# Performance work log

Measured on AMD Instinct MI355X. Metric: run time of the kernel, lower is better.

Reference implementation:

```python
import jax, jax.numpy as jnp
import numpy as np

N = 100000      # nodes
E = 3200000     # directed edges
IN = 512
H = 32          # hidden width fixed by the module
OUT = 64
EPS = 1e-5      # BatchNorm1d default eps


def setup_inputs() -> dict:
    key = jax.random.key(0)
    ks = jax.random.split(key, 10)
    x = jax.random.normal(ks[0], (N, IN), dtype=jnp.float32)
    edge_index = jax.random.randint(ks[1], (2, E), 0, N, dtype=jnp.int32)
    # GCNConv params (Linear weight + bias)
    W1 = jax.random.normal(ks[2], (IN, H), dtype=jnp.float32) / np.sqrt(IN)
    b1 = jnp.zeros((H,), dtype=jnp.float32)
    W2 = jax.random.normal(ks[3], (H, OUT), dtype=jnp.float32) / np.sqrt(H)
    b2 = jnp.zeros((OUT,), dtype=jnp.float32)
    # BatchNorm1d(32) params + running stats (eval mode)
    gamma = jax.random.normal(ks[4], (H,), dtype=jnp.float32) * 0.1 + 1.0
    beta = jax.random.normal(ks[5], (H,), dtype=jnp.float32) * 0.1
    running_mean = jax.random.normal(ks[6], (H,), dtype=jnp.float32) * 0.1
    running_var = jax.random.uniform(ks[7], (H,), dtype=jnp.float32, minval=0.5, maxval=1.5)
    return {"x": x, "edge_index": edge_index, "W1": W1, "b1": b1,
            "W2": W2, "b2": b2, "gamma": gamma, "beta": beta,
            "running_mean": running_mean, "running_var": running_var}


def _gcn_norm(edge_index):
    # PyG GCNConv default: add self-loops, symmetric normalization.
    src0, dst0 = edge_index[0], edge_index[1]
    loops = jnp.arange(N, dtype=edge_index.dtype)
    src = jnp.concatenate([src0, loops])
    dst = jnp.concatenate([dst0, loops])
    deg = jax.ops.segment_sum(jnp.ones_like(dst, dtype=jnp.float32), dst, num_segments=N)
    dinv = jnp.where(deg > 0, jax.lax.rsqrt(deg), 0.0)
    norm = dinv[src] * dinv[dst]  # [E+N]
    return src, dst, norm


def _gcn_conv(h, src, dst, norm, b):
    # gather -> scale -> scatter-add, then bias
    msg = h[src] * norm[:, None]
    agg = jax.ops.segment_sum(msg, dst, num_segments=N)
    return agg + b


def reference(x, edge_index, W1, b1, W2, b2, gamma, beta, running_mean, running_var):
    src, dst, norm = _gcn_norm(edge_index)
    h = _gcn_conv(x @ W1, src, dst, norm, b1)              # [N, 32]
    h = (h - running_mean) * jax.lax.rsqrt(running_var + EPS) * gamma + beta
    h = jax.nn.relu(h)
    # dropout is identity in eval mode
    out = _gcn_conv(h @ W2, src, dst, norm, b2)            # [N, 64]
    return out
```

## Files before the change

### kernel.cpp

```cpp
#include <hip/hip_runtime.h>
#include <hip/hip_fp16.h>

#define N_NODES 100000
#define E_EDGES 3200000
#define IN_F 512
#define H_F 32
#define OUT_F 64
#define BN_EPS 1e-5f
#define NBINS 1563
#define CHUNK 16384

struct H8 { __half2 h[4]; };
typedef _Float16 f16x8 __attribute__((ext_vector_type(8)));
typedef float    f32x4 __attribute__((ext_vector_type(4)));

__global__ __launch_bounds__(256) void k_prep(const float* __restrict__ gamma,
                                              const float* __restrict__ beta,
                                              const float* __restrict__ rm,
                                              const float* __restrict__ rv,
                                              const float* __restrict__ b1,
                                              float* __restrict__ scale,
                                              float* __restrict__ shift,
                                              unsigned* __restrict__ binCnt,
                                              unsigned* __restrict__ binPos) {
    int t = blockIdx.x * 256 + threadIdx.x;
    if (t < NBINS) { binCnt[t] = 0u; binPos[t] = 0u; }
    if (blockIdx.x == 0 && threadIdx.x < H_F) {
        int k = threadIdx.x;
        float s = gamma[k] * rsqrtf(rv[k] + BN_EPS);
        scale[k] = s;
        shift[k] = (b1[k] - rm[k]) * s + beta[k];
    }
}

__global__ __launch_bounds__(256) void k_wt(const float* __restrict__ W1,
                                            __half* __restrict__ w1t) {
    int t = blockIdx.x * 256 + threadIdx.x;
    if (t < IN_F * H_F) {
        int k = t >> 5, c = t & 31;
        w1t[c * IN_F + k] = __float2half(W1[t]);
    }
}

__global__ __launch_bounds__(256) void k_hist(const int* __restrict__ dst,
                                              unsigned* __restrict__ binCnt) {
    __shared__ unsigned h[NBINS];
    for (int i = threadIdx.x; i < NBINS; i += 256) h[i] = 0;
    __syncthreads();
    const int stride = 256 * 512;
    int e = blockIdx.x * 256 + threadIdx.x;
    for (; e + 3 * stride < E_EDGES; e += 4 * stride) {
        unsigned d0 = (unsigned)dst[e];
        unsigned d1 = (unsigned)dst[e + stride];
        unsigned d2 = (unsigned)dst[e + 2 * stride];
        unsigned d3 = (unsigned)dst[e + 3 * stride];
        atomicAdd(&h[d0 >> 6], 1u);
        atomicAdd(&h[d1 >> 6], 1u);
        atomicAdd(&h[d2 >> 6], 1u);
        atomicAdd(&h[d3 >> 6], 1u);
    }
    for (; e < E_EDGES; e += stride)
        atomicAdd(&h[((unsigned)dst[e]) >> 6], 1u);
    __syncthreads();
    for (int i = threadIdx.x; i < NBINS; i += 256) {
        unsigned v = h[i];
        if (v) atomicAdd(&binCnt[i], v);
    }
}

__global__ __launch_bounds__(256) void k_scanbins(const unsigned* __restrict__ binCnt,
                                                  unsigned* __restrict__ binOff) {
    __shared__ unsigned carry;
    __shared__ unsigned wtot[4];
    if (threadIdx.x == 0) carry = 0;
    __syncthreads();
    int lane = threadIdx.x & 63, wid = threadIdx.x >> 6;
    for (int base = 0; base < NBINS; base += 256) {
        int i = base + (int)threadIdx.x;
        unsigned v = (i < NBINS) ? binCnt[i] : 0u;
        unsigned xs = v;
#pragma unroll
        for (int s = 1; s < 64; s <<= 1) {
            unsigned t = __shfl_up(xs, s, 64);
            if (lane >= s) xs += t;
        }
        if (lane == 63) wtot[wid] = xs;
        __syncthreads();
        unsigned wbase = 0, tot = 0;
#pragma unroll
        for (int w = 0; w < 4; ++w) { if (w < wid) wbase += wtot[w]; tot += wtot[w]; }
        if (i < NBINS) binOff[i] = carry + wbase + xs - v;
        __syncthreads();
        if (threadIdx.x == 0) carry += tot;
        __syncthreads();
    }
}

__global__ __launch_bounds__(256) void k_binfill(const int* __restrict__ src,
                                                 const int* __restrict__ dst,
                                                 const unsigned* __restrict__ binOff,
                                                 unsigned* __restrict__ binPos,
                                                 unsigned* __restrict__ packed) {
    __shared__ unsigned h[NBINS];
    for (int i = threadIdx.x; i < NBINS; i += 256) h[i] = 0;
    __syncthreads();
    int e0 = blockIdx.x * CHUNK;
    int e1 = min(e0 + CHUNK, E_EDGES);
    for (int e = e0 + threadIdx.x; e < e1; e += 256)
        atomicAdd(&h[((unsigned)dst[e]) >> 6], 1u);
    __syncthreads();
    for (int i = threadIdx.x; i < NBINS; i += 256) {
        unsigned c = h[i];
        h[i] = c ? atomicAdd(&binPos[i], c) : 0u;
    }
    __syncthreads();
    for (int e = e0 + threadIdx.x; e < e1; e += 256) {
        unsigned s = (unsigned)src[e];
        unsigned d = (unsigned)dst[e];
        unsigned bin = d >> 6;
        unsigned pos = atomicAdd(&h[bin], 1u);
        packed[binOff[bin] + pos] = ((d & 63u) << 17) | s;
    }
}

__global__ __launch_bounds__(256) void k_sortbin(const unsigned* __restrict__ binOff,
                                                 const unsigned* __restrict__ binCnt,
                                                 const unsigned* __restrict__ packed,
                                                 unsigned* __restrict__ off,
                                                 unsigned* __restrict__ deg,
                                                 float* __restrict__ dinv,
                                                 unsigned* __restrict__ csr) {
    __shared__ unsigned cnt[64];
    __shared__ unsigned cur[64];
    int bin = blockIdx.x;
    if (threadIdx.x < 64) cnt[threadIdx.x] = 0;
    __syncthreads();
    unsigned base = binOff[bin], len = binCnt[bin];
    for (unsigned j = threadIdx.x; j < len; j += 256)
        atomicAdd(&cnt[packed[base + j] >> 17], 1u);
    __syncthreads();
    if (threadIdx.x < 64) {
        unsigned v = cnt[threadIdx.x];
        unsigned xs = v;
#pragma unroll
        for (int s = 1; s < 64; s <<= 1) {
            unsigned t = __shfl_up(xs, s, 64);
            if ((int)threadIdx.x >= s) xs += t;
        }
        unsigned loc = xs - v;
        cur[threadIdx.x] = loc;
        int node = bin * 64 + (int)threadIdx.x;
        if (node < N_NODES) {
            off[node]  = base + loc;
            deg[node]  = v;
            dinv[node] = rsqrtf((float)v + 1.0f);
        }
    }
    __syncthreads();
    for (unsigned j = threadIdx.x; j < len; j += 256) {
        unsigned p = packed[base + j];
        unsigned pos = atomicAdd(&cur[p >> 17], 1u);
        csr[base + pos] = p & 0x1FFFFu;
    }
}

__global__ __launch_bounds__(256) void k_gemm1(const float* __restrict__ x,
                                               const __half* __restrict__ w1t,
                                               const float* __restrict__ dinv,
                                               __half* __restrict__ xw16) {
    __shared__ _Float16 wsT[32][520];
    for (int i = threadIdx.x; i < 32 * 64; i += 256) {
        int c = i >> 6, k8 = i & 63;
        *(uint4*)&wsT[c][k8 * 8] = *(const uint4*)(w1t + c * IN_F + k8 * 8);
    }
    __syncthreads();

    const int wt = threadIdx.x >> 6;
    const int l  = threadIdx.x & 63;
    const int lr = l & 15;
    const int lk = l >> 4;
    const int row0 = blockIdx.x * 64 + wt * 16;
    int arow = row0 + lr;
    if (arow >= N_NODES) arow = N_NODES - 1;
    const float* xp = x + (size_t)arow * IN_F + lk * 8;

    f32x4 acc0 = {0.f, 0.f, 0.f, 0.f};
    f32x4 acc1 = {0.f, 0.f, 0.f, 0.f};
#pragma unroll 4
    for (int k0 = 0; k0 < IN_F; k0 += 32) {
        float4 xa = *(const float4*)(xp + k0);
        float4 xb = *(const float4*)(xp + k0 + 4);
        f16x8 a;
        a[0] = (_Float16)xa.x; a[1] = (_Float16)xa.y;
        a[2] = (_Float16)xa.z; a[3] = (_Float16)xa.w;
        a[4] = (_Float16)xb.x; a[5] = (_Float16)xb.y;
        a[6] = (_Float16)xb.z; a[7] = (_Float16)xb.w;
        f16x8 b0 = *(const f16x8*)&wsT[lr][k0 + lk * 8];
        f16x8 b1 = *(const f16x8*)&wsT[16 + lr][k0 + lk * 8];
        acc0 = __builtin_amdgcn_mfma_f32_16x16x32_f16(a, b0, acc0, 0, 0, 0);
        acc1 = __builtin_amdgcn_mfma_f32_16x16x32_f16(a, b1, acc1, 0, 0, 0);
    }
#pragma unroll
    for (int r = 0; r < 4; ++r) {
        int orow = row0 + lk * 4 + r;
        if (orow < N_NODES) {
            float dv = dinv[orow];
            xw16[(size_t)orow * H_F + lr]      = __float2half(acc0[r] * dv);
            xw16[(size_t)orow * H_F + 16 + lr] = __float2half(acc1[r] * dv);
        }
    }
}

__device__ inline void acc8(float* acc, float4 raw) {
    const __half2* h = (const __half2*)&raw;
#pragma unroll
    for (int j = 0; j < 4; ++j) {
        float2 f = __half22float2(h[j]);
        acc[2 * j]     += f.x;
        acc[2 * j + 1] += f.y;
    }
}

__global__ __launch_bounds__(256) void k_gather1(const unsigned* __restrict__ off,
                                                 const unsigned* __restrict__ deg,
                                                 const unsigned* __restrict__ csr,
                                                 const __half* __restrict__ xw16,
                                                 const float* __restrict__ dinv,
                                                 const float* __restrict__ scale,
                                                 const float* __restrict__ shift,
                                                 __half* __restrict__ hs16) {
    int lane  = threadIdx.x & 63;
    int ll    = lane & 31;
    int g     = ll >> 2;
    int q     = ll & 3;
    int d = blockIdx.x * 8 + ((threadIdx.x >> 6) << 1) + (lane >> 5);
    const unsigned* cp = csr + off[d];
    unsigned n = deg[d];
    float acc[8] = {};
    unsigned i = g;
    for (; i + 24 < n; i += 32) {
        unsigned s0 = cp[i], s1 = cp[i + 8], s2 = cp[i + 16], s3 = cp[i + 24];
        float4 r0 = *(const float4*)(xw16 + (size_t)s0 * H_F + q * 8);
        float4 r1 = *(const float4*)(xw16 + (size_t)s1 * H_F + q * 8);
        float4 r2 = *(const float4*)(xw16 + (size_t)s2 * H_F + q * 8);
        float4 r3 = *(const float4*)(xw16 + (size_t)s3 * H_F + q * 8);
        acc8(acc, r0); acc8(acc, r1); acc8(acc, r2); acc8(acc, r3);
    }
    for (; i < n; i += 8) {
        float4 r = *(const float4*)(xw16 + (size_t)cp[i] * H_F + q * 8);
        acc8(acc, r);
    }
#pragma unroll
    for (int st = 4; st <= 16; st <<= 1)
#pragma unroll
        for (int j = 0; j < 8; ++j)
            acc[j] += __shfl_xor(acc[j], st, 64);
    if (g == 0) {
        float dv = dinv[d];
        float sf[8];
        {
            float4 raw = *(const float4*)(xw16 + (size_t)d * H_F + q * 8);
            const __half2* h = (const __half2*)&raw;
#pragma unroll
            for (int j = 0; j < 4; ++j) {
                float2 f = __half22float2(h[j]);
                sf[2 * j] = f.x; sf[2 * j + 1] = f.y;
            }
        }
        float scf[8], shf[8];
        *(float4*)scf       = *(const float4*)(scale + q * 8);
        *(float4*)(scf + 4) = *(const float4*)(scale + q * 8 + 4);
        *(float4*)shf       = *(const float4*)(shift + q * 8);
        *(float4*)(shf + 4) = *(const float4*)(shift + q * 8 + 4);
        H8 o;
#pragma unroll
        for (int j = 0; j < 4; ++j) {
            float a0 = (acc[2 * j]     + sf[2 * j])     * dv;
            float a1 = (acc[2 * j + 1] + sf[2 * j + 1]) * dv;
            float h0 = fmaxf(fmaf(a0, scf[2 * j],     shf[2 * j]),     0.f) * dv;
            float h1 = fmaxf(fmaf(a1, scf[2 * j + 1], shf[2 * j + 1]), 0.f) * dv;
            o.h[j] = __floats2half2_rn(h0, h1);
        }
        *(H8*)(hs16 + (size_t)d * H_F + q * 8) = o;
    }
}

__global__ __launch_bounds__(256) void k_gather2(const unsigned* __restrict__ off,
                                                 const unsigned* __restrict__ deg,
                                                 const unsigned* __restrict__ csr,
                                                 const __half* __restrict__ hs16,
                                                 const float* __restrict__ dinv,
                                                 const float* __restrict__ W2,
                                                 const float* __restrict__ b2,
                                                 float* __restrict__ out) {
    __shared__ float ws[H_F * OUT_F];
    __shared__ float bs[OUT_F];
    for (int i = threadIdx.x; i < H_F * OUT_F; i += 256) ws[i] = W2[i];
    if (threadIdx.x < OUT_F) bs[threadIdx.x] = b2[threadIdx.x];
    __syncthreads();
    int lane  = threadIdx.x & 63;
    int ll    = lane & 31;
    int g     = ll >> 2;
    int q     = ll & 3;
    int d = blockIdx.x * 8 + ((threadIdx.x >> 6) << 1) + (lane >> 5);
    const unsigned* cp = csr + off[d];
    unsigned n = deg[d];
    float acc[8] = {};
    unsigned i = g;
    for (; i + 24 < n; i += 32) {
        unsigned s0 = cp[i], s1 = cp[i + 8], s2 = cp[i + 16], s3 = cp[i + 24];
        float4 r0 = *(const float4*)(hs16 + (size_t)s0 * H_F + q * 8);
        float4 r1 = *(const float4*)(hs16 + (size_t)s1 * H_F + q * 8);
        float4 r2 = *(const float4*)(hs16 + (size_t)s2 * H_F + q * 8);
        float4 r3 = *(const float4*)(hs16 + (size_t)s3 * H_F + q * 8);
        acc8(acc, r0); acc8(acc, r1); acc8(acc, r2); acc8(acc, r3);
    }
    for (; i < n; i += 8) {
        float4 r = *(const float4*)(hs16 + (size_t)cp[i] * H_F + q * 8);
        acc8(acc, r);
    }
#pragma unroll
    for (int st = 4; st <= 16; st <<= 1)
#pragma unroll
        for (int j = 0; j < 8; ++j)
            acc[j] += __shfl_xor(acc[j], st, 64);
    float tv[8];
#pragma unroll
    for (int j = 0; j < 8; ++j) tv[j] = 0.f;
    if (g == 0) {
        float dv = dinv[d];
        float4 raw = *(const float4*)(hs16 + (size_t)d * H_F + q * 8);
        const __half2* h = (const __half2*)&raw;
#pragma unroll
        for (int j = 0; j < 4; ++j) {
            float2 f = __half22float2(h[j]);
            tv[2 * j]     = (acc[2 * j]     + f.x) * dv;
            tv[2 * j + 1] = (acc[2 * j + 1] + f.y) * dv;
        }
    }
    float o0 = bs[ll], o1 = bs[ll + 32];
#pragma unroll
    for (int k = 0; k < H_F; ++k) {
        float a = __shfl(tv[k & 7], k >> 3, 32);
        o0 = fmaf(a, ws[k * OUT_F + ll],      o0);
        o1 = fmaf(a, ws[k * OUT_F + ll + 32], o1);
    }
    out[(size_t)d * OUT_F + ll]      = o0;
    out[(size_t)d * OUT_F + ll + 32] = o1;
}

extern "C" void kernel_launch(void* const* d_in, const int* in_sizes, int n_in,
                              void* d_out, int out_size, void* d_ws, size_t ws_size,
                              hipStream_t stream) {
    const float* x     = (const float*)d_in[0];
    const int*   ei    = (const int*)d_in[1];
    const float* W1    = (const float*)d_in[2];
    const float* b1    = (const float*)d_in[3];
    const float* W2    = (const float*)d_in[4];
    const float* b2    = (const float*)d_in[5];
    const float* gamma = (const float*)d_in[6];
    const float* beta  = (const float*)d_in[7];
    const float* rm    = (const float*)d_in[8];
    const float* rv    = (const float*)d_in[9];
    float* out = (float*)d_out;

    const int* src = ei;
    const int* dst = ei + E_EDGES;

    __half*   xw16   = (__half*)d_ws;
    __half*   hs16   = xw16 + (size_t)N_NODES * H_F;
    unsigned* packed = (unsigned*)d_ws;
    unsigned* csr    = (unsigned*)(hs16 + (size_t)N_NODES * H_F);
    float*    dinv   = (float*)(csr + E_EDGES);
    unsigned* off    = (unsigned*)(dinv + N_NODES);
    unsigned* deg    = off + N_NODES;
    float*    scale  = (float*)(deg + N_NODES);
    float*    shift  = scale + H_F;
    unsigned* binCnt = (unsigned*)(shift + H_F);
    unsigned* binPos = binCnt + NBINS;
    unsigned* binOff = binPos + NBINS;
    __half*   w1t    = (__half*)(binOff + NBINS);

    k_prep<<<(NBINS + 255) / 256, 256, 0, stream>>>(gamma, beta, rm, rv, b1,
                                                    scale, shift, binCnt, binPos);
    k_wt<<<(IN_F * H_F + 255) / 256, 256, 0, stream>>>(W1, w1t);
    k_hist<<<512, 256, 0, stream>>>(dst, binCnt);
    k_scanbins<<<1, 256, 0, stream>>>(binCnt, binOff);
    k_binfill<<<(E_EDGES + CHUNK - 1) / CHUNK, 256, 0, stream>>>(src, dst, binOff, binPos, packed);
    k_sortbin<<<NBINS, 256, 0, stream>>>(binOff, binCnt, packed, off, deg, dinv, csr);

    k_gemm1<<<(N_NODES + 63) / 64, 256, 0, stream>>>(x, w1t, dinv, xw16);
    k_gather1<<<N_NODES / 8, 256, 0, stream>>>(off, deg, csr, xw16, dinv, scale, shift, hs16);
    k_gather2<<<N_NODES / 8, 256, 0, stream>>>(off, deg, csr, hs16, dinv, W2, b2, out);
}
```

Before: 291.6 us.

## Run GEMM1 concurrently with edge binning in one fused launch, defer dinv scaling

Merges the x@W1 MFMA GEMM and the edge bin-fill pass into one heterogeneous kernel whose block ranges do different work. The bandwidth-heavy GEMM (reading x) can then overlap with the atomic-heavy binning instead of waiting for the CSR build to finish. The dinv row scaling moves out of the GEMM epilogue into k_sortbin, which rescales xw16 in place once degrees are known. It also folds the W1 transpose into k_prep, halves CHUNK, and moves packed to its own workspace region so it no longer aliases xw16. The trade-offs are extra workspace, a second read-modify-write pass over xw16, and shared-memory use sized for both roles, which may lower occupancy.

Result: no change. 288.5 us (-1.1%).

```diff
diff --git a/kernel.cpp b/kernel.cpp
--- a/kernel.cpp
+++ b/kernel.cpp
@@ -8,7 +8,9 @@
 #define OUT_F 64
 #define BN_EPS 1e-5f
 #define NBINS 1563
-#define CHUNK 16384
+#define CHUNK 8192
+#define NGB 1563
+#define NFB ((E_EDGES + CHUNK - 1) / CHUNK)
 
 struct H8 { __half2 h[4]; };
 typedef _Float16 f16x8 __attribute__((ext_vector_type(8)));
@@ -19,26 +21,23 @@
                                               const float* __restrict__ rm,
                                               const float* __restrict__ rv,
                                               const float* __restrict__ b1,
+                                              const float* __restrict__ W1,
                                               float* __restrict__ scale,
                                               float* __restrict__ shift,
                                               unsigned* __restrict__ binCnt,
-                                              unsigned* __restrict__ binPos) {
+                                              unsigned* __restrict__ binPos,
+                                              __half* __restrict__ w1t) {
     int t = blockIdx.x * 256 + threadIdx.x;
+    if (t < IN_F * H_F) {
+        int k = t >> 5, c = t & 31;
+        w1t[c * IN_F + k] = __float2half(W1[t]);
+    }
     if (t < NBINS) { binCnt[t] = 0u; binPos[t] = 0u; }
     if (blockIdx.x == 0 && threadIdx.x < H_F) {
         int k = threadIdx.x;
         float s = gamma[k] * rsqrtf(rv[k] + BN_EPS);
         scale[k] = s;
         shift[k] = (b1[k] - rm[k]) * s + beta[k];
-    }
-}
-
-__global__ __launch_bounds__(256) void k_wt(const float* __restrict__ W1,
-                                            __half* __restrict__ w1t) {
-    int t = blockIdx.x * 256 + threadIdx.x;
-    if (t < IN_F * H_F) {
-        int k = t >> 5, c = t & 31;
-        w1t[c * IN_F + k] = __float2half(W1[t]);
     }
 }
 
@@ -96,30 +95,78 @@
     }
 }
 
-__global__ __launch_bounds__(256) void k_binfill(const int* __restrict__ src,
-                                                 const int* __restrict__ dst,
-                                                 const unsigned* __restrict__ binOff,
-                                                 unsigned* __restrict__ binPos,
-                                                 unsigned* __restrict__ packed) {
+__global__ __launch_bounds__(256) void k_big(const float* __restrict__ x,
+                                             const __half* __restrict__ w1t,
+                                             __half* __restrict__ xw16,
+                                             const int* __restrict__ src,
+                                             const int* __restrict__ dst,
+                                             const unsigned* __restrict__ binOff,
+                                             unsigned* __restrict__ binPos,
+                                             unsigned* __restrict__ packed) {
+    __shared__ _Float16 wsT[32][520];
     __shared__ unsigned h[NBINS];
-    for (int i = threadIdx.x; i < NBINS; i += 256) h[i] = 0;
-    __syncthreads();
-    int e0 = blockIdx.x * CHUNK;
-    int e1 = min(e0 + CHUNK, E_EDGES);
-    for (int e = e0 + threadIdx.x; e < e1; e += 256)
-        atomicAdd(&h[((unsigned)dst[e]) >> 6], 1u);
-    __syncthreads();
-    for (int i = threadIdx.x; i < NBINS; i += 256) {
-        unsigned c = h[i];
-        h[i] = c ? atomicAdd(&binPos[i], c) : 0u;
-    }
-    __syncthreads();
-    for (int e = e0 + threadIdx.x; e < e1; e += 256) {
-        unsigned s = (unsigned)src[e];
-        unsigned d = (unsigned)dst[e];
-        unsigned bin = d >> 6;
-        unsigned pos = atomicAdd(&h[bin], 1u);
-        packed[binOff[bin] + pos] = ((d & 63u) << 17) | s;
+
+    if (blockIdx.x < NGB) {
+        for (int i = threadIdx.x; i < 32 * 64; i += 256) {
+            int c = i >> 6, k8 = i & 63;
+            *(uint4*)&wsT[c][k8 * 8] = *(const uint4*)(w1t + c * IN_F + k8 * 8);
+        }
+        __syncthreads();
+
+        const int wt = threadIdx.x >> 6;
+        const int l  = threadIdx.x & 63;
+        const int lr = l & 15;
+        const int lk = l >> 4;
+        const int row0 = blockIdx.x * 64 + wt * 16;
+        int arow = row0 + lr;
+        if (arow >= N_NODES) arow = N_NODES - 1;
+        const float* xp = x + (size_t)arow * IN_F + lk * 8;
+
+        f32x4 acc0 = {0.f, 0.f, 0.f, 0.f};
+        f32x4 acc1 = {0.f, 0.f, 0.f, 0.f};
+#pragma unroll 4
+        for (int k0 = 0; k0 < IN_F; k0 += 32) {
+            float4 xa = *(const float4*)(xp + k0);
+            float4 xb = *(const float4*)(xp + k0 + 4);
+            f16x8 a;
+            a[0] = (_Float16)xa.x; a[1] = (_Float16)xa.y;
+            a[2] = (_Float16)xa.z; a[3] = (_Float16)xa.w;
+            a[4] = (_Float16)xb.x; a[5] = (_Float16)xb.y;
+            a[6] = (_Float16)xb.z; a[7] = (_Float16)xb.w;
+            f16x8 b0 = *(const f16x8*)&wsT[lr][k0 + lk * 8];
+            f16x8 b1 = *(const f16x8*)&wsT[16 + lr][k0 + lk * 8];
+            acc0 = __builtin_amdgcn_mfma_f32_16x16x32_f16(a, b0, acc0, 0, 0, 0);
+            acc1 = __builtin_amdgcn_mfma_f32_16x16x32_f16(a, b1, acc1, 0, 0, 0);
+        }
+#pragma unroll
+        for (int r = 0; r < 4; ++r) {
+            int orow = row0 + lk * 4 + r;
+            if (orow < N_NODES) {
+                xw16[(size_t)orow * H_F + lr]      = __float2half(acc0[r]);
+                xw16[(size_t)orow * H_F + 16 + lr] = __float2half(acc1[r]);
+            }
+        }
+    } else {
+        for (int i = threadIdx.x; i < NBINS; i += 256) h[i] = 0;
+        __syncthreads();
+        int chunk = blockIdx.x - NGB;
+        int e0 = chunk * CHUNK;
+        int e1 = min(e0 + CHUNK, E_EDGES);
+        for (int e = e0 + threadIdx.x; e < e1; e += 256)
+            atomicAdd(&h[((unsigned)dst[e]) >> 6], 1u);
+        __syncthreads();
+        for (int i = threadIdx.x; i < NBINS; i += 256) {
+            unsigned c = h[i];
+            h[i] = c ? atomicAdd(&binPos[i], c) : 0u;
+        }
+        __syncthreads();
+        for (int e = e0 + threadIdx.x; e < e1; e += 256) {
+            unsigned s = (unsigned)src[e];
+            unsigned d = (unsigned)dst[e];
+            unsigned bin = d >> 6;
+            unsigned pos = atomicAdd(&h[bin], 1u);
+            packed[binOff[bin] + pos] = ((d & 63u) << 17) | s;
+        }
     }
 }
 
@@ -129,7 +176,8 @@
                                                  unsigned* __restrict__ off,
                                                  unsigned* __restrict__ deg,
                                                  float* __restrict__ dinv,
-                                                 unsigned* __restrict__ csr) {
+                                                 unsigned* __restrict__ csr,
+                                                 __half* __restrict__ xw16) {
     __shared__ unsigned cnt[64];
     __shared__ unsigned cur[64];
     int bin = blockIdx.x;
@@ -157,57 +205,25 @@
         }
     }
     __syncthreads();
+    {
+        int nl = threadIdx.x >> 2;
+        int c8 = (threadIdx.x & 3) * 8;
+        int node = bin * 64 + nl;
+        if (node < N_NODES) {
+            float dv = rsqrtf((float)cnt[nl] + 1.0f);
+            H8 v = *(H8*)(xw16 + (size_t)node * H_F + c8);
+#pragma unroll
+            for (int j = 0; j < 4; ++j) {
+                float2 f = __half22float2(v.h[j]);
+                v.h[j] = __floats2half2_rn(f.x * dv, f.y * dv);
+            }
+            *(H8*)(xw16 + (size_t)node * H_F + c8) = v;
+        }
+    }
     for (unsigned j = threadIdx.x; j < len; j += 256) {
         unsigned p = packed[base + j];
         unsigned pos = atomicAdd(&cur[p >> 17], 1u);
         csr[base + pos] = p & 0x1FFFFu;
-    }
-}
-
-__global__ __launch_bounds__(256) void k_gemm1(const float* __restrict__ x,
-                                               const __half* __restrict__ w1t,
-                                               const float* __restrict__ dinv,
-                                               __half* __restrict__ xw16) {
-    __shared__ _Float16 wsT[32][520];
-    for (int i = threadIdx.x; i < 32 * 64; i += 256) {
-        int c = i >> 6, k8 = i & 63;
-        *(uint4*)&wsT[c][k8 * 8] = *(const uint4*)(w1t + c * IN_F + k8 * 8);
-    }
-    __syncthreads();
-
-    const int wt = threadIdx.x >> 6;
-    const int l  = threadIdx.x & 63;
-    const int lr = l & 15;
-    const int lk = l >> 4;
-    const int row0 = blockIdx.x * 64 + wt * 16;
-    int arow = row0 + lr;
-    if (arow >= N_NODES) arow = N_NODES - 1;
-    const float* xp = x + (size_t)arow * IN_F + lk * 8;
-
-    f32x4 acc0 = {0.f, 0.f, 0.f, 0.f};
-    f32x4 acc1 = {0.f, 0.f, 0.f, 0.f};
-#pragma unroll 4
-    for (int k0 = 0; k0 < IN_F; k0 += 32) {
-        float4 xa = *(const float4*)(xp + k0);
-        float4 xb = *(const float4*)(xp + k0 + 4);
-        f16x8 a;
-        a[0] = (_Float16)xa.x; a[1] = (_Float16)xa.y;
-        a[2] = (_Float16)xa.z; a[3] = (_Float16)xa.w;
-        a[4] = (_Float16)xb.x; a[5] = (_Float16)xb.y;
-        a[6] = (_Float16)xb.z; a[7] = (_Float16)xb.w;
-        f16x8 b0 = *(const f16x8*)&wsT[lr][k0 + lk * 8];
-        f16x8 b1 = *(const f16x8*)&wsT[16 + lr][k0 + lk * 8];
-        acc0 = __builtin_amdgcn_mfma_f32_16x16x32_f16(a, b0, acc0, 0, 0, 0);
-        acc1 = __builtin_amdgcn_mfma_f32_16x16x32_f16(a, b1, acc1, 0, 0, 0);
-    }
-#pragma unroll
-    for (int r = 0; r < 4; ++r) {
-        int orow = row0 + lk * 4 + r;
-        if (orow < N_NODES) {
-            float dv = dinv[orow];
-            xw16[(size_t)orow * H_F + lr]      = __float2half(acc0[r] * dv);
-            xw16[(size_t)orow * H_F + 16 + lr] = __float2half(acc1[r] * dv);
-        }
     }
 }
 
@@ -369,9 +385,9 @@
 
     __half*   xw16   = (__half*)d_ws;
     __half*   hs16   = xw16 + (size_t)N_NODES * H_F;
-    unsigned* packed = (unsigned*)d_ws;
     unsigned* csr    = (unsigned*)(hs16 + (size_t)N_NODES * H_F);
-    float*    dinv   = (float*)(csr + E_EDGES);
+    unsigned* packed = csr + E_EDGES;
+    float*    dinv   = (float*)(packed + E_EDGES);
     unsigned* off    = (unsigned*)(dinv + N_NODES);
     unsigned* deg    = off + N_NODES;
     float*    scale  = (float*)(deg + N_NODES);
@@ -381,15 +397,13 @@
     unsigned* binOff = binPos + NBINS;
     __half*   w1t    = (__half*)(binOff + NBINS);
 
-    k_prep<<<(NBINS + 255) / 256, 256, 0, stream>>>(gamma, beta, rm, rv, b1,
-                                                    scale, shift, binCnt, binPos);
-    k_wt<<<(IN_F * H_F + 255) / 256, 256, 0, stream>>>(W1, w1t);
+    k_prep<<<64, 256, 0, stream>>>(gamma, beta, rm, rv, b1, W1,
+                                   scale, shift, binCnt, binPos, w1t);
     k_hist<<<512, 256, 0, stream>>>(dst, binCnt);
     k_scanbins<<<1, 256, 0, stream>>>(binCnt, binOff);
-    k_binfill<<<(E_EDGES + CHUNK - 1) / CHUNK, 256, 0, stream>>>(src, dst, binOff, binPos, packed);
-    k_sortbin<<<NBINS, 256, 0, stream>>>(binOff, binCnt, packed, off, deg, dinv, csr);
-
-    k_gemm1<<<(N_NODES + 63) / 64, 256, 0, stream>>>(x, w1t, dinv, xw16);
+    k_big<<<NGB + NFB, 256, 0, stream>>>(x, w1t, xw16, src, dst, binOff, binPos, packed);
+    k_sortbin<<<NBINS, 256, 0, stream>>>(binOff, binCnt, packed, off, deg, dinv, csr, xw16);
+
     k_gather1<<<N_NODES / 8, 256, 0, stream>>>(off, deg, csr, xw16, dinv, scale, shift, hs16);
     k_gather2<<<N_NODES / 8, 256, 0, stream>>>(off, deg, csr, hs16, dinv, W2, b2, out);
 }
```
